# Kernel optimization log

Measured on AMD Instinct MI355X. Metric: run time of the kernel, lower is better.

## Reference

```python
import jax, jax.numpy as jnp
import numpy as np

V, A, L = 10000, 600, 6          # dx vocab, num ancestors, ancestors-per-leaf
O, E = 128, 128                  # ontoEmbDim, EHREmbDim
ATD, PTD, DPL = 128, 128, 500    # ontoattnDim, ptattnDim, dpLabelSize
B, T, N = 64, 32, 40             # batch, visits, codes-per-visit


def _l2norm(x):
    return x / jnp.maximum(jnp.linalg.norm(x, axis=-1, keepdims=True), 1e-12)


def setup_inputs() -> dict:
    key = jax.random.key(0)
    ks = jax.random.split(key, 16)
    g = lambda k, shape, fan: (jax.random.normal(k, shape) / np.sqrt(fan)).astype(jnp.float32)
    dxseqs = jax.random.randint(ks[0], (B, T, N), 0, V + 1)          # V = padding idx
    dx_onehot = jax.random.uniform(ks[1], (T, B, V), dtype=jnp.float32)
    leaves = jax.random.randint(ks[2], (V, L), 0, V)
    ancestors = jax.random.randint(ks[3], (V, L), V, V + A)
    ehr_table = g(ks[4], (V + 1, E), E).at[V].set(0.0)               # padding row zero
    return dict(
        dxseqs=dxseqs, dx_onehot=dx_onehot, leaves=leaves, ancestors=ancestors,
        onto_table=g(ks[5], (V + A, O), O),
        onto_Wa=g(ks[6], (2 * O, ATD), 2 * O), onto_ba=jnp.zeros((ATD,), jnp.float32),
        onto_Wc=g(ks[7], (ATD, 1), ATD), onto_bc=jnp.zeros((1,), jnp.float32),
        ehr_table=ehr_table,
        attn_W=g(ks[8], (2 * E + 2 * O, PTD), 2 * E + 2 * O), attn_b=jnp.zeros((PTD,), jnp.float32),
        comb_W=g(ks[9], (PTD, 1), PTD), comb_b=jnp.zeros((1,), jnp.float32),
        co_W=g(ks[10], (E, V), E), co_b=jnp.zeros((V,), jnp.float32),
        dp_W=g(ks[11], (O + E, DPL), O + E), dp_b=jnp.zeros((DPL,), jnp.float32),
    )


def _forward(dxseqs, dx_onehot, leaves, ancestors, onto_table, onto_Wa, onto_ba,
             onto_Wc, onto_bc, ehr_table, attn_W, attn_b, comb_W, comb_b,
             co_W, co_b, dp_W, dp_b):
    # --- OntoEmb (GRAM-style ancestor attention) ---
    el = onto_table[leaves]                                  # (V, L, O)
    ea = onto_table[ancestors]                               # (V, L, O)
    h = jnp.tanh(jnp.concatenate([el, ea], -1) @ onto_Wa + onto_ba)
    a = jax.nn.softmax(h @ onto_Wc + onto_bc, axis=1)        # (V, L, 1)
    onto_all = jnp.concatenate(
        [jnp.sum(a * ea, axis=1), jnp.zeros((1, O), onto_table.dtype)], axis=0)  # (V+1, O)

    dxOnto = onto_all[dxseqs]                                # (B, T, N, O)
    ontoV = jnp.einsum('tbv,vo->bto', dx_onehot, onto_all[:-1])  # (B, T, O)
    dxEHR = ehr_table[dxseqs]                                # (B, T, N, E)
    ehrV = _l2norm(jnp.sum(dxEHR, axis=2))                   # (B, T, E)

    # --- cooccurrence branch ---
    cooccurU = jax.nn.softmax(ehrV @ co_W + co_b, axis=2)    # (B, T, V)
    vonehot = jnp.transpose(dx_onehot, (1, 0, 2))            # (B, T, V)
    cooccur_loss = -jnp.mean(jnp.sum(vonehot * jnp.log(cooccurU), axis=(1, 2)))

    # --- additive (Bahdanau) attention over codes in a visit ---
    dxEmb = jnp.concatenate([dxEHR, dxOnto], -1)             # (B, T, N, E+O)
    vs = jnp.concatenate([ontoV, ehrV], -1)[:, :, None, :]   # (B, T, 1, O+E)
    attnInput = jnp.concatenate([jnp.broadcast_to(vs, dxEmb.shape), dxEmb], -1)
    mlp = jnp.tanh(attnInput @ attn_W + attn_b)              # (B, T, N, PTD)
    attn = jax.nn.softmax(mlp @ comb_W + comb_b, axis=2)     # (B, T, N, 1)
    vs2 = jnp.sum(attn * dxEmb, axis=2)                      # (B, T, E+O)

    dp = jax.nn.softmax(jnp.tanh(_l2norm(vs2)) @ dp_W + dp_b, axis=2)  # (B, T, DPL)
    return dp, cooccur_loss * 10.0


def reference(dxseqs, dx_onehot, leaves, ancestors, onto_table, onto_Wa, onto_ba,
              onto_Wc, onto_bc, ehr_table, attn_W, attn_b, comb_W, comb_b,
              co_W, co_b, dp_W, dp_b):
    return _forward(dxseqs, dx_onehot, leaves, ancestors, onto_table, onto_Wa, onto_ba,
                    onto_Wc, onto_bc, ehr_table, attn_W, attn_b, comb_W, comb_b,
                    co_W, co_b, dp_W, dp_b)
```

## Files before the change

kernel.cpp:

```cpp
#include <hip/hip_runtime.h>
#include <math.h>

typedef float4 f4;
typedef __bf16 bf16x8 __attribute__((ext_vector_type(8)));
typedef float f32x4 __attribute__((ext_vector_type(4)));

static constexpr int kV = 10000, kL = 6, kDPL = 500;
static constexpr int kB = 64, kT = 32, kN = 40, kBT = 2048;
static constexpr int kXC = 5;
static constexpr int kNB = 272;
static constexpr int kLd = 10240;
static constexpr int kVT2 = 40;

#define MFMA16 __builtin_amdgcn_mfma_f32_16x16x32_bf16

typedef const __attribute__((address_space(1))) unsigned int ga_u32;
typedef __attribute__((address_space(3))) unsigned int lds_u32;
__device__ __forceinline__ void gll16(const float* g, float* l) {
  __builtin_amdgcn_global_load_lds((ga_u32*)g, (lds_u32*)l, 16, 0, 0);
}

__device__ __forceinline__ bf16x8 cvt8(f4 a, f4 b) {
  bf16x8 r;
  r[0] = (__bf16)a.x; r[1] = (__bf16)a.y; r[2] = (__bf16)a.z; r[3] = (__bf16)a.w;
  r[4] = (__bf16)b.x; r[5] = (__bf16)b.y; r[6] = (__bf16)b.z; r[7] = (__bf16)b.w;
  return r;
}

__global__ __launch_bounds__(256) void mmore_cvt_bf16(
    const float* __restrict__ in, __bf16* __restrict__ out, int n) {
  int i = (blockIdx.x * 256 + threadIdx.x) * 8;
  if (i < n) {
    f4 a = *(const f4*)(in + i), b = *(const f4*)(in + i + 4);
    *(bf16x8*)(out + i) = cvt8(a, b);
  }
}

__global__ __launch_bounds__(256) void mmore_trcvt(
    const float* __restrict__ in, __bf16* __restrict__ out,
    int K, int N, int Kpad) {
  int t = threadIdx.x;
  int n = blockIdx.y * 16 + (t & 15);
  int kb = (blockIdx.x * 16 + (t >> 4)) * 8;
  bf16x8 r;
  #pragma unroll
  for (int i = 0; i < 8; ++i) {
    int k = kb + i;
    float v = (k < K && n < N) ? in[(size_t)k * N + n] : 0.f;
    r[i] = (__bf16)v;
  }
  *(bf16x8*)(out + (size_t)n * Kpad + kb) = r;
}

__global__ __launch_bounds__(256) void mmore_brow(
    const float* __restrict__ coW, const float* __restrict__ cob,
    __bf16* __restrict__ Btab) {
  int id = blockIdx.x * 256 + threadIdx.x;
  int rr = id / 1280;
  int kk = (id - rr * 1280) * 8;
  bf16x8 r;
  #pragma unroll
  for (int i = 0; i < 8; ++i) {
    int k = kk + i;
    float v = 0.f;
    if (k < kV) {
      if (rr < 128) v = coW[(size_t)rr * kV + k];
      else if (rr == 128) v = cob[k];
      else if (rr == 129) v = 1.f;
    }
    r[i] = (__bf16)v;
  }
  *(bf16x8*)(Btab + (size_t)(128 + rr) * kLd + kk) = r;
}

__global__ __launch_bounds__(128) void mmore_ehrv(
    const int* __restrict__ dxseqs, const float* __restrict__ ehr_table,
    float* __restrict__ ehrV) {
  int bt = blockIdx.x, t = threadIdx.x;
  const int* row = dxseqs + bt * kN;
  float acc = 0.f;
  for (int n = 0; n < kN; ++n) acc += ehr_table[(size_t)row[n] * 128 + t];
  float v = acc * acc;
  #pragma unroll
  for (int off = 32; off; off >>= 1) v += __shfl_down(v, off);
  __shared__ float red[2];
  if ((t & 63) == 0) red[t >> 6] = v;
  __syncthreads();
  float ss = red[0] + red[1];
  float inv = 1.f / fmaxf(sqrtf(ss), 1e-12f);
  ehrV[bt * 128 + t] = acc * inv;
}

__global__ __launch_bounds__(256) void mmore_scores_mfma(
    const __bf16* __restrict__ otb, const int* __restrict__ leaves,
    const int* __restrict__ anc, const __bf16* __restrict__ WaT,
    const float* __restrict__ ba, const float* __restrict__ Wc,
    const float* __restrict__ bc, float* __restrict__ s_out) {
  int t = threadIdx.x, wave = t >> 6, lane = t & 63, lm = lane & 15, lg = lane >> 4;
  int r0 = blockIdx.x * 32;
  int rA0 = r0 + lm, rA1 = rA0 + 16;
  int v0 = rA0 / 6, l0 = rA0 - v0 * 6, v1 = rA1 / 6, l1 = rA1 - v1 * 6;
  const __bf16* pL0 = otb + (size_t)leaves[v0 * 6 + l0] * 128;
  const __bf16* pA0 = otb + (size_t)anc[v0 * 6 + l0] * 128;
  const __bf16* pL1 = otb + (size_t)leaves[v1 * 6 + l1] * 128;
  const __bf16* pA1 = otb + (size_t)anc[v1 * 6 + l1] * 128;
  const __bf16* bp = WaT + (size_t)(wave * 32 + lm) * 256 + lg * 8;
  f32x4 acc[2][2] = {};
  #pragma unroll
  for (int kb = 0; kb < 256; kb += 32) {
    int k = kb + lg * 8;
    const __bf16* s0 = (k < 128) ? (pL0 + k) : (pA0 + (k - 128));
    const __bf16* s1 = (k < 128) ? (pL1 + k) : (pA1 + (k - 128));
    bf16x8 a0 = *(const bf16x8*)s0;
    bf16x8 a1 = *(const bf16x8*)s1;
    bf16x8 b0 = *(const bf16x8*)(bp + kb);
    bf16x8 b1 = *(const bf16x8*)(bp + kb + 16 * 256);
    acc[0][0] = MFMA16(a0, b0, acc[0][0], 0, 0, 0);
    acc[0][1] = MFMA16(a0, b1, acc[0][1], 0, 0, 0);
    acc[1][0] = MFMA16(a1, b0, acc[1][0], 0, 0, 0);
    acc[1][1] = MFMA16(a1, b1, acc[1][1], 0, 0, 0);
  }
  __shared__ float red[4][32];
  float bcv = bc[0];
  #pragma unroll
  for (int mf = 0; mf < 2; ++mf) {
    #pragma unroll
    for (int j = 0; j < 4; ++j) {
      float p = 0.f;
      #pragma unroll
      for (int nf = 0; nf < 2; ++nf) {
        int c = wave * 32 + nf * 16 + lm;
        p += tanhf(acc[mf][nf][j] + ba[c]) * Wc[c];
      }
      #pragma unroll
      for (int off = 8; off; off >>= 1) p += __shfl_xor(p, off);
      if (lm == 0) red[wave][mf * 16 + lg * 4 + j] = p;
    }
  }
  __syncthreads();
  if (t < 32) s_out[r0 + t] = red[0][t] + red[1][t] + red[2][t] + red[3][t] + bcv;
}

__global__ __launch_bounds__(128) void mmore_onto(
    const float* __restrict__ ot, const int* __restrict__ anc,
    const float* __restrict__ s_in, float* __restrict__ onto_all) {
  int v = blockIdx.x, t = threadIdx.x;
  if (v == kV) { onto_all[(size_t)v * 128 + t] = 0.f; return; }
  __shared__ float sv[kL];
  __shared__ int aidx[kL];
  if (t < kL) { sv[t] = s_in[v * kL + t]; aidx[t] = anc[v * kL + t]; }
  __syncthreads();
  float mx = sv[0];
  #pragma unroll
  for (int l = 1; l < kL; ++l) mx = fmaxf(mx, sv[l]);
  float e[kL], sum = 0.f;
  #pragma unroll
  for (int l = 0; l < kL; ++l) { e[l] = expf(sv[l] - mx); sum += e[l]; }
  float acc = 0.f;
  #pragma unroll
  for (int l = 0; l < kL; ++l)
    acc += (e[l] / sum) * ot[(size_t)aidx[l] * 128 + t];
  onto_all[(size_t)v * 128 + t] = acc;
}

__global__ __launch_bounds__(512) void mmore_xgemm(
    const float* __restrict__ X, const __bf16* __restrict__ Btab,
    float* __restrict__ part) {
  __shared__ __align__(16) float a_s[3][16][32];
  int t = threadIdx.x, wid = t >> 6, lane = t & 63, lm = lane & 15, lg = lane >> 4;
  int btile = blockIdx.x & 127, chunk = blockIdx.x >> 7;
  int r0 = btile * 16, ko = chunk * 2048;
  int nsteps = (chunk < 4) ? 64 : 56;
  int srow = (wid << 3) + (lane >> 3);
  int sg = (lane & 7) ^ (((lane >> 3) & 3) << 1);
  const float* sptr = X + (size_t)(r0 + srow) * kV + ko + sg * 4;
  int q1 = (((lg * 2) ^ ((lm & 3) << 1))) << 2;
  const __bf16* bp0 = Btab + (size_t)(wid * 16 + lm) * kLd + ko + lg * 8;
  const __bf16* bp1 = bp0 + (size_t)128 * kLd;
  const __bf16* bp2 = Btab + (size_t)(256 + lm) * kLd + ko + lg * 8;
  f32x4 acc0 = {}, acc1 = {}, acc2 = {};
  if (wid < 2) {
    gll16(sptr, &a_s[0][wid * 8][0]);
    gll16(sptr + 32, &a_s[1][wid * 8][0]);
  }
  for (int s = 0; s < nsteps; ++s) {
    int cur = s % 3;
    if (wid < 2) {
      int s2 = s + 2;
      if (s2 < nsteps) gll16(sptr + (size_t)s2 * 32, &a_s[s2 % 3][wid * 8][0]);
      int pend = nsteps - 1 - s;
      if (pend >= 2)      asm volatile("s_waitcnt vmcnt(2)" ::: "memory");
      else if (pend == 1) asm volatile("s_waitcnt vmcnt(1)" ::: "memory");
      else                asm volatile("s_waitcnt vmcnt(0)" ::: "memory");
    }
    __builtin_amdgcn_s_barrier();
    asm volatile("" ::: "memory");
    f4 x0 = *(const f4*)&a_s[cur][lm][q1];
    f4 x1 = *(const f4*)&a_s[cur][lm][q1 + 4];
    bf16x8 af = cvt8(x0, x1);
    int kb = s * 32;
    bf16x8 b0 = *(const bf16x8*)(bp0 + kb);
    bf16x8 b1 = *(const bf16x8*)(bp1 + kb);
    acc0 = MFMA16(af, b0, acc0, 0, 0, 0);
    acc1 = MFMA16(af, b1, acc1, 0, 0, 0);
    if (wid == 0) {
      bf16x8 b2 = *(const bf16x8*)(bp2 + kb);
      acc2 = MFMA16(af, b2, acc2, 0, 0, 0);
    }
    asm volatile("" ::: "memory");
    __builtin_amdgcn_s_barrier();
  }
  if (chunk == 4) {
    __syncthreads();
    if (t < 128) {
      int r = t >> 3, g = t & 7;
      int sk = 9984 + ((g ^ ((r & 3) << 1)) << 2);
      f4 v = make_float4(0.f, 0.f, 0.f, 0.f);
      if (sk < kV) v = *(const f4*)(X + (size_t)(r0 + r) * kV + sk);
      *(f4*)&a_s[0][r][g * 4] = v;
    }
    __syncthreads();
    int kb = 56 * 32;
    f4 x0 = *(const f4*)&a_s[0][lm][q1];
    f4 x1 = *(const f4*)&a_s[0][lm][q1 + 4];
    bf16x8 af = cvt8(x0, x1);
    acc0 = MFMA16(af, *(const bf16x8*)(bp0 + kb), acc0, 0, 0, 0);
    acc1 = MFMA16(af, *(const bf16x8*)(bp1 + kb), acc1, 0, 0, 0);
    if (wid == 0) acc2 = MFMA16(af, *(const bf16x8*)(bp2 + kb), acc2, 0, 0, 0);
  }
  #pragma unroll
  for (int j = 0; j < 4; ++j) {
    int r = r0 + lg * 4 + j;
    int bt = (r & 63) * kT + (r >> 6);
    size_t o = ((size_t)chunk * kBT + bt) * kNB;
    part[o + wid * 16 + lm] = acc0[j];
    part[o + 128 + wid * 16 + lm] = acc1[j];
    if (wid == 0) part[o + 256 + lm] = acc2[j];
  }
}

__global__ __launch_bounds__(256) void mmore_creduce(
    const float* __restrict__ part, float* __restrict__ ontoV,
    float* __restrict__ pwred, float* __restrict__ pc, float* __restrict__ sp) {
  int bt = blockIdx.x, t = threadIdx.x;
  for (int c = t; c < kNB; c += 256) {
    float a = 0.f;
    #pragma unroll
    for (int ch = 0; ch < kXC; ++ch)
      a += part[((size_t)ch * kBT + bt) * kNB + c];
    if (c < 128) ontoV[(size_t)bt * 128 + c] = a;
    else if (c < 256) pwred[(size_t)bt * 128 + (c - 128)] = a;
    else if (c == 256) pc[bt] = a;
    else if (c == 257) sp[bt] = a;
  }
}

__global__ __launch_bounds__(256) void mmore_lossg(
    const float* __restrict__ ehrV, const __bf16* __restrict__ coWT,
    const float* __restrict__ cob, float* __restrict__ epart) {
  int t = threadIdx.x, wave = t >> 6, lane = t & 63, lm = lane & 15, lg = lane >> 4;
  int vt = blockIdx.x, btile = blockIdx.y;
  int r0 = btile * 32, vb = vt * 256;
  const float* a0 = ehrV + (size_t)(r0 + lm) * 128 + lg * 8;
  const float* a1 = a0 + 16 * 128;
  f32x4 acc[2][4] = {};
  #pragma unroll
  for (int kb = 0; kb < 128; kb += 32) {
    f4 x0 = *(const f4*)(a0 + kb), x1 = *(const f4*)(a0 + kb + 4);
    f4 y0 = *(const f4*)(a1 + kb), y1 = *(const f4*)(a1 + kb + 4);
    bf16x8 af0 = cvt8(x0, x1), af1 = cvt8(y0, y1);
    #pragma unroll
    for (int nf = 0; nf < 4; ++nf) {
      int c = vb + wave * 64 + nf * 16 + lm;
      bf16x8 b = *(const bf16x8*)(coWT + (size_t)c * 128 + kb + lg * 8);
      acc[0][nf] = MFMA16(af0, b, acc[0][nf], 0, 0, 0);
      acc[1][nf] = MFMA16(af1, b, acc[1][nf], 0, 0, 0);
    }
  }
  float se[2][4] = {};
  #pragma unroll
  for (int nf = 0; nf < 4; ++nf) {
    int c = vb + wave * 64 + nf * 16 + lm;
    if (c < kV) {
      float cb = cob[c];
      #pragma unroll
      for (int mf = 0; mf < 2; ++mf)
        #pragma unroll
        for (int j = 0; j < 4; ++j)
          se[mf][j] += __expf(acc[mf][nf][j] + cb);
    }
  }
  __shared__ float red[4][32];
  #pragma unroll
  for (int mf = 0; mf < 2; ++mf)
    #pragma unroll
    for (int j = 0; j < 4; ++j) {
      float v = se[mf][j];
      #pragma unroll
      for (int off = 8; off; off >>= 1) v += __shfl_xor(v, off);
      if (lm == 0) red[wave][mf * 16 + lg * 4 + j] = v;
    }
  __syncthreads();
  if (t < 32)
    epart[(size_t)vt * kBT + r0 + t] =
        red[0][t] + red[1][t] + red[2][t] + red[3][t];
}

__global__ __launch_bounds__(256) void mmore_lossterm(
    const float* __restrict__ ehrV, const float* __restrict__ pwred,
    const float* __restrict__ pc, const float* __restrict__ sp,
    const float* __restrict__ epart, float* __restrict__ term) {
  int t = threadIdx.x;
  int bt = blockIdx.x * 16 + (t >> 4);
  int sub = t & 15;
  const f4* e = (const f4*)(ehrV + (size_t)bt * 128 + sub * 8);
  const f4* w = (const f4*)(pwred + (size_t)bt * 128 + sub * 8);
  f4 e0 = e[0], e1 = e[1], w0 = w[0], w1 = w[1];
  float d = e0.x * w0.x + e0.y * w0.y + e0.z * w0.z + e0.w * w0.w +
            e1.x * w1.x + e1.y * w1.y + e1.z * w1.z + e1.w * w1.w;
  float S = 0.f;
  for (int vt = sub; vt < kVT2; vt += 16) S += epart[(size_t)vt * kBT + bt];
  #pragma unroll
  for (int off = 8; off; off >>= 1) {
    d += __shfl_xor(d, off); S += __shfl_xor(S, off);
  }
  if (sub == 0) term[bt] = (d + pc[bt]) - sp[bt] * logf(S);
}

__global__ __launch_bounds__(256) void mmore_lossfin(
    const float* __restrict__ term, float* __restrict__ out) {
  int t = threadIdx.x;
  float a = 0.f;
  for (int i = t; i < kBT; i += 256) a += term[i];
  #pragma unroll
  for (int off = 32; off; off >>= 1) a += __shfl_down(a, off);
  __shared__ float red[4];
  if ((t & 63) == 0) red[t >> 6] = a;
  __syncthreads();
  if (t == 0) out[0] = -(10.f / 64.f) * (red[0] + red[1] + red[2] + red[3]);
}

__global__ __launch_bounds__(256) void mmore_gemm_mfma(
    const float* __restrict__ A, const __bf16* __restrict__ WT,
    int ldWT, int koff, const float* __restrict__ bias,
    float* __restrict__ C, int M, int accumulate) {
  int t = threadIdx.x, wave = t >> 6, lane = t & 63, lm = lane & 15, lg = lane >> 4;
  int r0 = blockIdx.x * 32;
  int row0 = r0 + lm, row1 = row0 + 16;
  bool ok0 = row0 < M, ok1 = row1 < M;
  const float* a0 = A + (size_t)row0 * 128 + lg * 8;
  const float* a1 = A + (size_t)row1 * 128 + lg * 8;
  const __bf16* bp = WT + (size_t)(wave * 32 + lm) * ldWT + koff + lg * 8;
  int ld16 = 16 * ldWT;
  f32x4 acc[2][2] = {};
  #pragma unroll
  for (int kb = 0; kb < 128; kb += 32) {
    f4 x0 = make_float4(0, 0, 0, 0), x1 = x0, y0 = x0, y1 = x0;
    if (ok0) { x0 = *(const f4*)(a0 + kb); x1 = *(const f4*)(a0 + kb + 4); }
    if (ok1) { y0 = *(const f4*)(a1 + kb); y1 = *(const f4*)(a1 + kb + 4); }
    bf16x8 af0 = cvt8(x0, x1), af1 = cvt8(y0, y1);
    bf16x8 b0 = *(const bf16x8*)(bp + kb);
    bf16x8 b1 = *(const bf16x8*)(bp + kb + ld16);
    acc[0][0] = MFMA16(af0, b0, acc[0][0], 0, 0, 0);
    acc[0][1] = MFMA16(af0, b1, acc[0][1], 0, 0, 0);
    acc[1][0] = MFMA16(af1, b0, acc[1][0], 0, 0, 0);
    acc[1][1] = MFMA16(af1, b1, acc[1][1], 0, 0, 0);
  }
  #pragma unroll
  for (int mf = 0; mf < 2; ++mf)
    #pragma unroll
    for (int nf = 0; nf < 2; ++nf) {
      int col = wave * 32 + nf * 16 + lm;
      #pragma unroll
      for (int j = 0; j < 4; ++j) {
        int row = r0 + mf * 16 + lg * 4 + j;
        if (row < M) {
          float v = acc[mf][nf][j];
          if (bias) v += bias[col];
          if (accumulate) v += C[(size_t)row * 128 + col];
          C[(size_t)row * 128 + col] = v;
        }
      }
    }
}

__device__ __forceinline__ float mmore_block_sum(float v, float* red) {
  int t = threadIdx.x;
  #pragma unroll
  for (int off = 32; off; off >>= 1) v += __shfl_down(v, off);
  if ((t & 63) == 0) red[t >> 6] = v;
  __syncthreads();
  if (t == 0) red[0] = red[0] + red[1] + red[2] + red[3];
  __syncthreads();
  return red[0];
}

__global__ __launch_bounds__(256) void mmore_attn(
    const int* __restrict__ dxseqs, const float* __restrict__ base,
    const float* __restrict__ pe, const float* __restrict__ po,
    const float* __restrict__ combW, const float* __restrict__ combB,
    const float* __restrict__ ehr_table, const float* __restrict__ onto_all,
    float* __restrict__ tn) {
  __shared__ float base_s[128];
  __shared__ int idx_s[kN];
  __shared__ float scp[kN][2];
  __shared__ float attn_s[64];
  __shared__ float red[4];
  int bt = blockIdx.x, t = threadIdx.x;
  if (t < 128) base_s[t] = base[bt * 128 + t];
  if (t < kN) idx_s[t] = dxseqs[bt * kN + t];
  __syncthreads();
  int c = t & 127, half = t >> 7, wid = t >> 6, lane = t & 63;
  float cw = combW[c];
  for (int n2 = 0; n2 < kN / 2; ++n2) {
    int n = n2 * 2 + half;
    int id = idx_s[n];
    float x = base_s[c] + pe[(size_t)id * 128 + c] + po[(size_t)id * 128 + c];
    float val = tanhf(x) * cw;
    #pragma unroll
    for (int off = 32; off; off >>= 1) val += __shfl_down(val, off);
    if (lane == 0) scp[n][wid & 1] = val;
  }
  __syncthreads();
  if (t < 64) {
    float s = (t < kN) ? (scp[t][0] + scp[t][1] + combB[0]) : -1e30f;
    float mx = s;
    #pragma unroll
    for (int off = 32; off; off >>= 1) mx = fmaxf(mx, __shfl_xor(mx, off));
    float e = (t < kN) ? __expf(s - mx) : 0.f;
    float sm = e;
    #pragma unroll
    for (int off = 32; off; off >>= 1) sm += __shfl_xor(sm, off);
    attn_s[t] = e / sm;
  }
  __syncthreads();
  float acc = 0.f;
  {
    const float* tab = (t < 128) ? ehr_table : onto_all;
    int j = t & 127;
    for (int n = 0; n < kN; ++n)
      acc += attn_s[n] * tab[(size_t)idx_s[n] * 128 + j];
  }
  float ss = mmore_block_sum(acc * acc, red);
  float inv = 1.f / fmaxf(sqrtf(ss), 1e-12f);
  tn[(size_t)bt * 256 + t] = tanhf(acc * inv);
}

__global__ __launch_bounds__(256) void mmore_dpgemm(
    const float* __restrict__ tn, const __bf16* __restrict__ dpWT,
    const float* __restrict__ dpB, float* __restrict__ u) {
  int t = threadIdx.x, wave = t >> 6, lane = t & 63, lm = lane & 15, lg = lane >> 4;
  int c0 = blockIdx.x * 128, r0 = blockIdx.y * 32;
  const float* a0 = tn + (size_t)(r0 + lm) * 256 + lg * 8;
  const float* a1 = a0 + 16 * 256;
  const __bf16* bp = dpWT + (size_t)(c0 + wave * 32 + lm) * 256 + lg * 8;
  f32x4 acc[2][2] = {};
  #pragma unroll
  for (int kb = 0; kb < 256; kb += 32) {
    f4 x0 = *(const f4*)(a0 + kb), x1 = *(const f4*)(a0 + kb + 4);
    f4 y0 = *(const f4*)(a1 + kb), y1 = *(const f4*)(a1 + kb + 4);
    bf16x8 af0 = cvt8(x0, x1), af1 = cvt8(y0, y1);
    bf16x8 b0 = *(const bf16x8*)(bp + kb);
    bf16x8 b1 = *(const bf16x8*)(bp + kb + 16 * 256);
    acc[0][0] = MFMA16(af0, b0, acc[0][0], 0, 0, 0);
    acc[0][1] = MFMA16(af0, b1, acc[0][1], 0, 0, 0);
    acc[1][0] = MFMA16(af1, b0, acc[1][0], 0, 0, 0);
    acc[1][1] = MFMA16(af1, b1, acc[1][1], 0, 0, 0);
  }
  #pragma unroll
  for (int mf = 0; mf < 2; ++mf)
    #pragma unroll
    for (int nf = 0; nf < 2; ++nf) {
      int col = c0 + wave * 32 + nf * 16 + lm;
      float bias = (col < kDPL) ? dpB[col] : 0.f;
      #pragma unroll
      for (int j = 0; j < 4; ++j) {
        int row = r0 + mf * 16 + lg * 4 + j;
        u[(size_t)row * 512 + col] = acc[mf][nf][j] + bias;
      }
    }
}

__global__ __launch_bounds__(128) void mmore_dpsoft(
    const float* __restrict__ u, float* __restrict__ out) {
  int bt = blockIdx.x, t = threadIdx.x;
  __shared__ float red[2];
  float v[4]; float mx = -1e30f;
  #pragma unroll
  for (int i = 0; i < 4; ++i) {
    int c = t + i * 128;
    v[i] = (c < kDPL) ? u[(size_t)bt * 512 + c] : -1e30f;
    mx = fmaxf(mx, v[i]);
  }
  #pragma unroll
  for (int off = 32; off; off >>= 1) mx = fmaxf(mx, __shfl_xor(mx, off));
  if ((t & 63) == 0) red[t >> 6] = mx;
  __syncthreads();
  mx = fmaxf(red[0], red[1]);
  __syncthreads();
  float e[4], s = 0.f;
  #pragma unroll
  for (int i = 0; i < 4; ++i) {
    int c = t + i * 128;
    e[i] = (c < kDPL) ? __expf(v[i] - mx) : 0.f;
    s += e[i];
  }
  #pragma unroll
  for (int off = 32; off; off >>= 1) s += __shfl_xor(s, off);
  if ((t & 63) == 0) red[t >> 6] = s;
  __syncthreads();
  float invS = 1.f / (red[0] + red[1]);
  #pragma unroll
  for (int i = 0; i < 4; ++i) {
    int c = t + i * 128;
    if (c < kDPL) out[(size_t)bt * kDPL + c] = e[i] * invS;
  }
}

extern "C" void kernel_launch(void* const* d_in, const int* in_sizes, int n_in,
                              void* d_out, int out_size, void* d_ws, size_t ws_size,
                              hipStream_t stream) {
  const int*   dxseqs     = (const int*)d_in[0];
  const float* dx_onehot  = (const float*)d_in[1];
  const int*   leaves     = (const int*)d_in[2];
  const int*   ancestors  = (const int*)d_in[3];
  const float* onto_table = (const float*)d_in[4];
  const float* onto_Wa    = (const float*)d_in[5];
  const float* onto_ba    = (const float*)d_in[6];
  const float* onto_Wc    = (const float*)d_in[7];
  const float* onto_bc    = (const float*)d_in[8];
  const float* ehr_table  = (const float*)d_in[9];
  const float* attn_W     = (const float*)d_in[10];
  const float* attn_b     = (const float*)d_in[11];
  const float* comb_W     = (const float*)d_in[12];
  const float* comb_b     = (const float*)d_in[13];
  const float* co_W       = (const float*)d_in[14];
  const float* co_b       = (const float*)d_in[15];
  const float* dp_W       = (const float*)d_in[16];
  const float* dp_b       = (const float*)d_in[17];
  float* out = (float*)d_out;

  float* ws = (float*)d_ws;
  size_t off = 0;
  auto alloc = [&](size_t n) { float* p = ws + off; off += n; return p; };
  float* onto_all = alloc((size_t)(kV + 1) * 128);
  float* s_sc     = alloc((size_t)kV * kL);
  float* ehrV     = alloc((size_t)kBT * 128);
  float* ontoV    = alloc((size_t)kBT * 128);
  __bf16* Btab    = (__bf16*)alloc((size_t)kNB * kLd / 2);
  __bf16* attn_WT = (__bf16*)alloc((size_t)128 * 512 / 2);
  __bf16* dpWT    = (__bf16*)alloc((size_t)512 * 256 / 2);
  __bf16* WaT     = (__bf16*)alloc((size_t)128 * 256 / 2);
  float* peR      = alloc((size_t)(kV + 1) * 128);
  float* poR      = alloc((size_t)(kV + 1) * 128);
  float* basep    = alloc((size_t)kBT * 128);
  float* epart    = alloc((size_t)kVT2 * kBT);
  float* pwred    = alloc((size_t)kBT * 128);
  float* pc       = alloc(kBT);
  float* sp       = alloc(kBT);
  float* term     = alloc(kBT);
  __bf16* ot_bf = (__bf16*)peR;
  float*  cpart = peR;
  __bf16* coWT  = (__bf16*)peR;
  float*  u     = peR;
  float*  tn    = ehrV;

  mmore_cvt_bf16<<<663, 256, 0, stream>>>(onto_table, ot_bf, 10600 * 128);
  mmore_trcvt<<<dim3(2, 8), 256, 0, stream>>>(onto_Wa, WaT, 256, 128, 256);
  mmore_trcvt<<<dim3(4, 8), 256, 0, stream>>>(attn_W, attn_WT, 512, 128, 512);
  mmore_trcvt<<<dim3(2, 32), 256, 0, stream>>>(dp_W, dpWT, 256, kDPL, 256);

  mmore_ehrv<<<kBT, 128, 0, stream>>>(dxseqs, ehr_table, ehrV);
  mmore_scores_mfma<<<(kV * kL) / 32, 256, 0, stream>>>(
      ot_bf, leaves, ancestors, WaT, onto_ba, onto_Wc, onto_bc, s_sc);
  mmore_onto<<<kV + 1, 128, 0, stream>>>(onto_table, ancestors, s_sc, onto_all);
  mmore_trcvt<<<dim3(80, 8), 256, 0, stream>>>(onto_all, Btab, kV, 128, kLd);
  mmore_brow<<<720, 256, 0, stream>>>(co_W, co_b, Btab);
  mmore_xgemm<<<128 * kXC, 512, 0, stream>>>(dx_onehot, Btab, cpart);
  mmore_creduce<<<kBT, 256, 0, stream>>>(cpart, ontoV, pwred, pc, sp);
  mmore_trcvt<<<dim3(1, 640), 256, 0, stream>>>(co_W, coWT, 128, kV, 128);
  mmore_lossg<<<dim3(kVT2, 64), 256, 0, stream>>>(ehrV, coWT, co_b, epart);
  mmore_lossterm<<<kBT / 16, 256, 0, stream>>>(ehrV, pwred, pc, sp, epart, term);
  mmore_lossfin<<<1, 256, 0, stream>>>(term, out + (size_t)kBT * kDPL);
  mmore_gemm_mfma<<<313, 256, 0, stream>>>(ehr_table, attn_WT, 512, 256, nullptr, peR, kV + 1, 0);
  mmore_gemm_mfma<<<313, 256, 0, stream>>>(onto_all, attn_WT, 512, 384, nullptr, poR, kV + 1, 0);
  mmore_gemm_mfma<<<64, 256, 0, stream>>>(ontoV, attn_WT, 512, 0, nullptr, basep, kBT, 0);
  mmore_gemm_mfma<<<64, 256, 0, stream>>>(ehrV, attn_WT, 512, 128, attn_b, basep, kBT, 1);
  mmore_attn<<<kBT, 256, 0, stream>>>(dxseqs, basep, peR, poR, comb_W, comb_b,
                                      ehr_table, onto_all, tn);
  mmore_dpgemm<<<dim3(4, 64), 256, 0, stream>>>(tn, dpWT, dp_b, u);
  mmore_dpsoft<<<kBT, 128, 0, stream>>>(u, out);
}
```

Before: 315.1 us.

## Retile dx one-hot GEMM to 32-row tiles with intra-block split-K and double buffering

Rewrites the main X·Btab GEMM so each block handles 32 rows instead of 16. Each of 8 waves computes a 16x128 output slab over half of the K chunk (intra-block split-K), and the halves are reduced through LDS before the partials are written. A-tile staging now uses 128-wide K stages with double buffering, loaded by all threads instead of two waves. The larger tile reuses each Btab fragment across twice as many rows and cuts per-step barrier overhead. In exchange it uses more LDS and registers, adds an LDS reduction step, and halves the grid to 320 blocks.

```diff
diff --git a/kernel.cpp b/kernel.cpp
--- a/kernel.cpp
+++ b/kernel.cpp
@@ -163,79 +163,122 @@
   onto_all[(size_t)v * 128 + t] = acc;
 }
 
+#define XG_STAGE(db, s)                                                       \
+  {                                                                           \
+    int kk0_ = kbase + (s) * 128;                                             \
+    _Pragma("unroll")                                                         \
+    for (int u = 0; u < 4; ++u) {                                             \
+      int row_ = u * 8 + g * 2 + s_sub;                                       \
+      int sg_ = (s_gr & 24) | ((s_gr ^ row_) & 7);                            \
+      gll16(X + (size_t)(r0 + row_) * kV + kk0_ + sg_ * 4,                    \
+            &a_s[kh][db][u * 1024 + g * 256]);                                \
+    }                                                                         \
+  }
+
+#define XG_CSTEP(db, s)                                                       \
+  {                                                                           \
+    const __bf16* bs_ = bbase + (s) * 128;                                    \
+    _Pragma("unroll")                                                         \
+    for (int kk = 0; kk < 4; ++kk) {                                          \
+      f4 x0_ = *(const f4*)&a_s[kh][db][roff[kk][0]];                         \
+      f4 x1_ = *(const f4*)&a_s[kh][db][roff[kk][1]];                         \
+      bf16x8 af_ = cvt8(x0_, x1_);                                            \
+      _Pragma("unroll")                                                       \
+      for (int nf = 0; nf < 8; ++nf) {                                        \
+        bf16x8 b_ = *(const bf16x8*)(bs_ + (size_t)(f0 + nf) * 16 * kLd + kk * 32); \
+        acc[nf] = MFMA16(af_, b_, acc[nf], 0, 0, 0);                          \
+      }                                                                       \
+      if (nh) {                                                               \
+        bf16x8 b_ = *(const bf16x8*)(bs_ + (size_t)256 * kLd + kk * 32);      \
+        acc8 = MFMA16(af_, b_, acc8, 0, 0, 0);                                \
+      }                                                                       \
+    }                                                                         \
+  }
+
 __global__ __launch_bounds__(512) void mmore_xgemm(
     const float* __restrict__ X, const __bf16* __restrict__ Btab,
     float* __restrict__ part) {
-  __shared__ __align__(16) float a_s[3][16][32];
-  int t = threadIdx.x, wid = t >> 6, lane = t & 63, lm = lane & 15, lg = lane >> 4;
-  int btile = blockIdx.x & 127, chunk = blockIdx.x >> 7;
-  int r0 = btile * 16, ko = chunk * 2048;
-  int nsteps = (chunk < 4) ? 64 : 56;
-  int srow = (wid << 3) + (lane >> 3);
-  int sg = (lane & 7) ^ (((lane >> 3) & 3) << 1);
-  const float* sptr = X + (size_t)(r0 + srow) * kV + ko + sg * 4;
-  int q1 = (((lg * 2) ^ ((lm & 3) << 1))) << 2;
-  const __bf16* bp0 = Btab + (size_t)(wid * 16 + lm) * kLd + ko + lg * 8;
-  const __bf16* bp1 = bp0 + (size_t)128 * kLd;
-  const __bf16* bp2 = Btab + (size_t)(256 + lm) * kLd + ko + lg * 8;
-  f32x4 acc0 = {}, acc1 = {}, acc2 = {};
-  if (wid < 2) {
-    gll16(sptr, &a_s[0][wid * 8][0]);
-    gll16(sptr + 32, &a_s[1][wid * 8][0]);
-  }
+  __shared__ __align__(16) float a_s[2][2][32 * 128];
+  int t = threadIdx.x;
+  int w = t >> 6, lane = t & 63, lm = lane & 15, lg = lane >> 4;
+  int kh = w >> 2, mf = (w >> 1) & 1, nh = w & 1, g = w & 3;
+  int btile = blockIdx.x & 63, chunk = blockIdx.x >> 6;
+  int r0 = btile * 32;
+  bool lastc = (chunk == kXC - 1);
+  int kbase = lastc ? (8192 + kh * 896) : (chunk * 2048 + kh * 1024);
+  int nsteps = lastc ? 7 : 8;
+  int arow = mf * 16 + lm;
+  int f0 = nh * 8;
+  int s_sub = lane >> 5, s_gr = lane & 31;
+  const __bf16* bbase = Btab + (size_t)lm * kLd + kbase + lg * 8;
+  int roff[4][2];
+  #pragma unroll
+  for (int kk = 0; kk < 4; ++kk)
+    #pragma unroll
+    for (int h = 0; h < 2; ++h) {
+      int G = kk * 8 + lg * 2 + h;
+      int gl = (G & 24) | ((G ^ arow) & 7);
+      roff[kk][h] = arow * 128 + gl * 4;
+    }
+  f32x4 acc[8] = {};
+  f32x4 acc8 = {};
+
+  XG_STAGE(0, 0);
+  __syncthreads();
+  int db = 0;
   for (int s = 0; s < nsteps; ++s) {
-    int cur = s % 3;
-    if (wid < 2) {
-      int s2 = s + 2;
-      if (s2 < nsteps) gll16(sptr + (size_t)s2 * 32, &a_s[s2 % 3][wid * 8][0]);
-      int pend = nsteps - 1 - s;
-      if (pend >= 2)      asm volatile("s_waitcnt vmcnt(2)" ::: "memory");
-      else if (pend == 1) asm volatile("s_waitcnt vmcnt(1)" ::: "memory");
-      else                asm volatile("s_waitcnt vmcnt(0)" ::: "memory");
-    }
+    if (s + 1 < nsteps) XG_STAGE(db ^ 1, s + 1);
+    XG_CSTEP(db, s);
+    asm volatile("s_waitcnt vmcnt(0)" ::: "memory");
     __builtin_amdgcn_s_barrier();
-    asm volatile("" ::: "memory");
-    f4 x0 = *(const f4*)&a_s[cur][lm][q1];
-    f4 x1 = *(const f4*)&a_s[cur][lm][q1 + 4];
+    db ^= 1;
+  }
+  if (lastc && kh == 1) {
+    f4 z = make_float4(0.f, 0.f, 0.f, 0.f), x0 = z, x1 = z;
+    if (lg < 2) {
+      const float* xp = X + (size_t)(r0 + arow) * kV + 9984 + lg * 8;
+      x0 = *(const f4*)xp; x1 = *(const f4*)(xp + 4);
+    }
     bf16x8 af = cvt8(x0, x1);
-    int kb = s * 32;
-    bf16x8 b0 = *(const bf16x8*)(bp0 + kb);
-    bf16x8 b1 = *(const bf16x8*)(bp1 + kb);
-    acc0 = MFMA16(af, b0, acc0, 0, 0, 0);
-    acc1 = MFMA16(af, b1, acc1, 0, 0, 0);
-    if (wid == 0) {
-      bf16x8 b2 = *(const bf16x8*)(bp2 + kb);
-      acc2 = MFMA16(af, b2, acc2, 0, 0, 0);
-    }
-    asm volatile("" ::: "memory");
-    __builtin_amdgcn_s_barrier();
-  }
-  if (chunk == 4) {
-    __syncthreads();
-    if (t < 128) {
-      int r = t >> 3, g = t & 7;
-      int sk = 9984 + ((g ^ ((r & 3) << 1)) << 2);
-      f4 v = make_float4(0.f, 0.f, 0.f, 0.f);
-      if (sk < kV) v = *(const f4*)(X + (size_t)(r0 + r) * kV + sk);
-      *(f4*)&a_s[0][r][g * 4] = v;
-    }
-    __syncthreads();
-    int kb = 56 * 32;
-    f4 x0 = *(const f4*)&a_s[0][lm][q1];
-    f4 x1 = *(const f4*)&a_s[0][lm][q1 + 4];
-    bf16x8 af = cvt8(x0, x1);
-    acc0 = MFMA16(af, *(const bf16x8*)(bp0 + kb), acc0, 0, 0, 0);
-    acc1 = MFMA16(af, *(const bf16x8*)(bp1 + kb), acc1, 0, 0, 0);
-    if (wid == 0) acc2 = MFMA16(af, *(const bf16x8*)(bp2 + kb), acc2, 0, 0, 0);
-  }
-  #pragma unroll
-  for (int j = 0; j < 4; ++j) {
-    int r = r0 + lg * 4 + j;
-    int bt = (r & 63) * kT + (r >> 6);
-    size_t o = ((size_t)chunk * kBT + bt) * kNB;
-    part[o + wid * 16 + lm] = acc0[j];
-    part[o + 128 + wid * 16 + lm] = acc1[j];
-    if (wid == 0) part[o + 256 + lm] = acc2[j];
+    const __bf16* bs = Btab + (size_t)lm * kLd + 9984 + lg * 8;
+    #pragma unroll
+    for (int nf = 0; nf < 8; ++nf) {
+      bf16x8 b = *(const bf16x8*)(bs + (size_t)(f0 + nf) * 16 * kLd);
+      acc[nf] = MFMA16(af, b, acc[nf], 0, 0, 0);
+    }
+    if (nh) {
+      bf16x8 b = *(const bf16x8*)(bs + (size_t)256 * kLd);
+      acc8 = MFMA16(af, b, acc8, 0, 0, 0);
+    }
+  }
+  __syncthreads();
+  float* red = &a_s[0][0][0];
+  if (kh == 1) {
+    #pragma unroll
+    for (int nf = 0; nf < 8; ++nf)
+      #pragma unroll
+      for (int j = 0; j < 4; ++j)
+        red[(mf * 16 + lg * 4 + j) * kNB + (f0 + nf) * 16 + lm] = acc[nf][j];
+    if (nh)
+      #pragma unroll
+      for (int j = 0; j < 4; ++j)
+        red[(mf * 16 + lg * 4 + j) * kNB + 256 + lm] = acc8[j];
+  }
+  __syncthreads();
+  if (kh == 0) {
+    #pragma unroll
+    for (int j = 0; j < 4; ++j) {
+      int row = mf * 16 + lg * 4 + j;
+      int r = r0 + row;
+      int bt = (r & 63) * kT + (r >> 6);
+      size_t o = ((size_t)chunk * kBT + bt) * kNB;
+      #pragma unroll
+      for (int nf = 0; nf < 8; ++nf) {
+        int col = (f0 + nf) * 16 + lm;
+        part[o + col] = acc[nf][j] + red[row * kNB + col];
+      }
+      if (nh) part[o + 256 + lm] = acc8[j] + red[row * kNB + 256 + lm];
+    }
   }
 }
 
@@ -576,7 +619,7 @@
   mmore_onto<<<kV + 1, 128, 0, stream>>>(onto_table, ancestors, s_sc, onto_all);
   mmore_trcvt<<<dim3(80, 8), 256, 0, stream>>>(onto_all, Btab, kV, 128, kLd);
   mmore_brow<<<720, 256, 0, stream>>>(co_W, co_b, Btab);
-  mmore_xgemm<<<128 * kXC, 512, 0, stream>>>(dx_onehot, Btab, cpart);
+  mmore_xgemm<<<64 * kXC, 512, 0, stream>>>(dx_onehot, Btab, cpart);
   mmore_creduce<<<kBT, 256, 0, stream>>>(cpart, ontoV, pwred, pc, sp);
   mmore_trcvt<<<dim3(1, 640), 256, 0, stream>>>(co_W, coWT, 128, kV, 128);
   mmore_lossg<<<dim3(kVT2, 64), 256, 0, stream>>>(ehrV, coWT, co_b, epart);
```

After: 357.1 us. +13.3%, slower.

## Panelize B table and drop LDS staging in dx one-hot GEMM

Applied to the files above, without the earlier changes.

Adds a panelize kernel that rearranges the bf16 B table into contiguous 32-wide k-panels so each MFMA step reads a compact block of B. The xgemm kernel drops the LDS triple buffer, its barriers and the async global-to-LDS loads, and instead reads the A operand directly from global memory into registers. It also halves the block size to 256 threads, gives each wave five accumulators, and swizzles the block order. The goal is to remove barrier stalls and improve B locality, at the cost of one extra launch and an extra pass over the B table.

```diff
diff --git a/kernel.cpp b/kernel.cpp
--- a/kernel.cpp
+++ b/kernel.cpp
@@ -10,15 +10,10 @@
 static constexpr int kXC = 5;
 static constexpr int kNB = 272;
 static constexpr int kLd = 10240;
+static constexpr int kNP = 313;
 static constexpr int kVT2 = 40;
 
 #define MFMA16 __builtin_amdgcn_mfma_f32_16x16x32_bf16
-
-typedef const __attribute__((address_space(1))) unsigned int ga_u32;
-typedef __attribute__((address_space(3))) unsigned int lds_u32;
-__device__ __forceinline__ void gll16(const float* g, float* l) {
-  __builtin_amdgcn_global_load_lds((ga_u32*)g, (lds_u32*)l, 16, 0, 0);
-}
 
 __device__ __forceinline__ bf16x8 cvt8(f4 a, f4 b) {
   bf16x8 r;
@@ -71,6 +66,15 @@
     r[i] = (__bf16)v;
   }
   *(bf16x8*)(Btab + (size_t)(128 + rr) * kLd + kk) = r;
+}
+
+__global__ __launch_bounds__(256) void mmore_panelize(
+    const __bf16* __restrict__ Btab, __bf16* __restrict__ Bp) {
+  int t = threadIdx.x;
+  int S = blockIdx.x, ry = blockIdx.y;
+  int row = ry * 16 + (t >> 4), kk = (t & 15) * 2;
+  unsigned v = *(const unsigned*)(Btab + (size_t)row * kLd + S * 32 + kk);
+  *(unsigned*)(Bp + ((size_t)S * kNB + row) * 32 + kk) = v;
 }
 
 __global__ __launch_bounds__(128) void mmore_ehrv(
@@ -163,79 +167,56 @@
   onto_all[(size_t)v * 128 + t] = acc;
 }
 
-__global__ __launch_bounds__(512) void mmore_xgemm(
-    const float* __restrict__ X, const __bf16* __restrict__ Btab,
+__global__ __launch_bounds__(256) void mmore_xgemm(
+    const float* __restrict__ X, const __bf16* __restrict__ Bp,
     float* __restrict__ part) {
-  __shared__ __align__(16) float a_s[3][16][32];
-  int t = threadIdx.x, wid = t >> 6, lane = t & 63, lm = lane & 15, lg = lane >> 4;
-  int btile = blockIdx.x & 127, chunk = blockIdx.x >> 7;
-  int r0 = btile * 16, ko = chunk * 2048;
-  int nsteps = (chunk < 4) ? 64 : 56;
-  int srow = (wid << 3) + (lane >> 3);
-  int sg = (lane & 7) ^ (((lane >> 3) & 3) << 1);
-  const float* sptr = X + (size_t)(r0 + srow) * kV + ko + sg * 4;
-  int q1 = (((lg * 2) ^ ((lm & 3) << 1))) << 2;
-  const __bf16* bp0 = Btab + (size_t)(wid * 16 + lm) * kLd + ko + lg * 8;
-  const __bf16* bp1 = bp0 + (size_t)128 * kLd;
-  const __bf16* bp2 = Btab + (size_t)(256 + lm) * kLd + ko + lg * 8;
-  f32x4 acc0 = {}, acc1 = {}, acc2 = {};
-  if (wid < 2) {
-    gll16(sptr, &a_s[0][wid * 8][0]);
-    gll16(sptr + 32, &a_s[1][wid * 8][0]);
-  }
+  int t = threadIdx.x, w = t >> 6, lane = t & 63, lm = lane & 15, lg = lane >> 4;
+  int bid = blockIdx.x;
+  int swz = (bid & 7) * 80 + (bid >> 3);
+  int btile = swz & 127, chunk = swz >> 7;
+  int r0 = btile * 16;
+  bool lastc = (chunk == kXC - 1);
+  int nsteps = lastc ? 56 : 64;
+  int f0 = w * 4;
+  const float* ap = X + (size_t)(r0 + lm) * kV + chunk * 2048 + lg * 8;
+  const __bf16* bp = Bp + ((size_t)(chunk * 64) * kNB + lm) * 32 + lg * 8;
+  f32x4 acc[5] = {};
+  #pragma unroll 4
   for (int s = 0; s < nsteps; ++s) {
-    int cur = s % 3;
-    if (wid < 2) {
-      int s2 = s + 2;
-      if (s2 < nsteps) gll16(sptr + (size_t)s2 * 32, &a_s[s2 % 3][wid * 8][0]);
-      int pend = nsteps - 1 - s;
-      if (pend >= 2)      asm volatile("s_waitcnt vmcnt(2)" ::: "memory");
-      else if (pend == 1) asm volatile("s_waitcnt vmcnt(1)" ::: "memory");
-      else                asm volatile("s_waitcnt vmcnt(0)" ::: "memory");
-    }
-    __builtin_amdgcn_s_barrier();
-    asm volatile("" ::: "memory");
-    f4 x0 = *(const f4*)&a_s[cur][lm][q1];
-    f4 x1 = *(const f4*)&a_s[cur][lm][q1 + 4];
+    f4 x0 = *(const f4*)(ap + s * 32);
+    f4 x1 = *(const f4*)(ap + s * 32 + 4);
     bf16x8 af = cvt8(x0, x1);
-    int kb = s * 32;
-    bf16x8 b0 = *(const bf16x8*)(bp0 + kb);
-    bf16x8 b1 = *(const bf16x8*)(bp1 + kb);
-    acc0 = MFMA16(af, b0, acc0, 0, 0, 0);
-    acc1 = MFMA16(af, b1, acc1, 0, 0, 0);
-    if (wid == 0) {
-      bf16x8 b2 = *(const bf16x8*)(bp2 + kb);
-      acc2 = MFMA16(af, b2, acc2, 0, 0, 0);
-    }
-    asm volatile("" ::: "memory");
-    __builtin_amdgcn_s_barrier();
-  }
-  if (chunk == 4) {
-    __syncthreads();
-    if (t < 128) {
-      int r = t >> 3, g = t & 7;
-      int sk = 9984 + ((g ^ ((r & 3) << 1)) << 2);
-      f4 v = make_float4(0.f, 0.f, 0.f, 0.f);
-      if (sk < kV) v = *(const f4*)(X + (size_t)(r0 + r) * kV + sk);
-      *(f4*)&a_s[0][r][g * 4] = v;
-    }
-    __syncthreads();
-    int kb = 56 * 32;
-    f4 x0 = *(const f4*)&a_s[0][lm][q1];
-    f4 x1 = *(const f4*)&a_s[0][lm][q1 + 4];
+    const __bf16* bs = bp + (size_t)s * (kNB * 32);
+    acc[0] = MFMA16(af, *(const bf16x8*)(bs + (f0 + 0) * 512), acc[0], 0, 0, 0);
+    acc[1] = MFMA16(af, *(const bf16x8*)(bs + (f0 + 1) * 512), acc[1], 0, 0, 0);
+    acc[2] = MFMA16(af, *(const bf16x8*)(bs + (f0 + 2) * 512), acc[2], 0, 0, 0);
+    acc[3] = MFMA16(af, *(const bf16x8*)(bs + (f0 + 3) * 512), acc[3], 0, 0, 0);
+    if (w == 3)
+      acc[4] = MFMA16(af, *(const bf16x8*)(bs + 16 * 512), acc[4], 0, 0, 0);
+  }
+  if (lastc) {
+    f4 z = make_float4(0.f, 0.f, 0.f, 0.f), x0 = z, x1 = z;
+    if (lg < 2) {
+      x0 = *(const f4*)(ap + 56 * 32);
+      x1 = *(const f4*)(ap + 56 * 32 + 4);
+    }
     bf16x8 af = cvt8(x0, x1);
-    acc0 = MFMA16(af, *(const bf16x8*)(bp0 + kb), acc0, 0, 0, 0);
-    acc1 = MFMA16(af, *(const bf16x8*)(bp1 + kb), acc1, 0, 0, 0);
-    if (wid == 0) acc2 = MFMA16(af, *(const bf16x8*)(bp2 + kb), acc2, 0, 0, 0);
+    const __bf16* bs = bp + (size_t)56 * (kNB * 32);
+    acc[0] = MFMA16(af, *(const bf16x8*)(bs + (f0 + 0) * 512), acc[0], 0, 0, 0);
+    acc[1] = MFMA16(af, *(const bf16x8*)(bs + (f0 + 1) * 512), acc[1], 0, 0, 0);
+    acc[2] = MFMA16(af, *(const bf16x8*)(bs + (f0 + 2) * 512), acc[2], 0, 0, 0);
+    acc[3] = MFMA16(af, *(const bf16x8*)(bs + (f0 + 3) * 512), acc[3], 0, 0, 0);
+    if (w == 3)
+      acc[4] = MFMA16(af, *(const bf16x8*)(bs + 16 * 512), acc[4], 0, 0, 0);
   }
   #pragma unroll
   for (int j = 0; j < 4; ++j) {
     int r = r0 + lg * 4 + j;
     int bt = (r & 63) * kT + (r >> 6);
     size_t o = ((size_t)chunk * kBT + bt) * kNB;
-    part[o + wid * 16 + lm] = acc0[j];
-    part[o + 128 + wid * 16 + lm] = acc1[j];
-    if (wid == 0) part[o + 256 + lm] = acc2[j];
+    #pragma unroll
+    for (int f = 0; f < 4; ++f) part[o + (f0 + f) * 16 + lm] = acc[f][j];
+    if (w == 3) part[o + 256 + lm] = acc[4][j];
   }
 }
 
@@ -547,7 +528,7 @@
   float* s_sc     = alloc((size_t)kV * kL);
   float* ehrV     = alloc((size_t)kBT * 128);
   float* ontoV    = alloc((size_t)kBT * 128);
-  __bf16* Btab    = (__bf16*)alloc((size_t)kNB * kLd / 2);
+  __bf16* Bp      = (__bf16*)alloc((size_t)kNP * kNB * 32 / 2);
   __bf16* attn_WT = (__bf16*)alloc((size_t)128 * 512 / 2);
   __bf16* dpWT    = (__bf16*)alloc((size_t)512 * 256 / 2);
   __bf16* WaT     = (__bf16*)alloc((size_t)128 * 256 / 2);
@@ -560,6 +541,7 @@
   float* sp       = alloc(kBT);
   float* term     = alloc(kBT);
   __bf16* ot_bf = (__bf16*)peR;
+  __bf16* BtabL = (__bf16*)peR;
   float*  cpart = peR;
   __bf16* coWT  = (__bf16*)peR;
   float*  u     = peR;
@@ -574,9 +556,10 @@
   mmore_scores_mfma<<<(kV * kL) / 32, 256, 0, stream>>>(
       ot_bf, leaves, ancestors, WaT, onto_ba, onto_Wc, onto_bc, s_sc);
   mmore_onto<<<kV + 1, 128, 0, stream>>>(onto_table, ancestors, s_sc, onto_all);
-  mmore_trcvt<<<dim3(80, 8), 256, 0, stream>>>(onto_all, Btab, kV, 128, kLd);
-  mmore_brow<<<720, 256, 0, stream>>>(co_W, co_b, Btab);
-  mmore_xgemm<<<128 * kXC, 512, 0, stream>>>(dx_onehot, Btab, cpart);
+  mmore_trcvt<<<dim3(80, 8), 256, 0, stream>>>(onto_all, BtabL, kV, 128, kLd);
+  mmore_brow<<<720, 256, 0, stream>>>(co_W, co_b, BtabL);
+  mmore_panelize<<<dim3(kNP, 17), 256, 0, stream>>>(BtabL, Bp);
+  mmore_xgemm<<<128 * kXC, 256, 0, stream>>>(dx_onehot, Bp, cpart);
   mmore_creduce<<<kBT, 256, 0, stream>>>(cpart, ontoV, pwred, pc, sp);
   mmore_trcvt<<<dim3(1, 640), 256, 0, stream>>>(co_W, coWT, 128, kV, 128);
   mmore_lossg<<<dim3(kVT2, 64), 256, 0, stream>>>(ehrV, coWT, co_b, epart);
```

New measurement: 304.6 us. 1.03x faster.
